# Optimization experiments

Measured on AMD Instinct MI355X. Metric: run time of the kernel, lower is better.

The kernel has to match this reference:

```python
import jax, jax.numpy as jnp
import numpy as np

B, S, D, H = 2, 2048, 1024, 16
HD = D // H  # head dim = 64


def setup_inputs() -> dict:
    key = jax.random.key(0)
    ks = jax.random.split(key, 11)
    s = 0.02
    return {
        "query": jax.random.normal(ks[0], (B, S, D), jnp.float32),
        "key": jax.random.normal(ks[1], (B, S, D), jnp.float32),
        "value": jax.random.normal(ks[2], (B, S, D), jnp.float32),
        "Wq": jax.random.normal(ks[3], (D, D), jnp.float32) * s,
        "bq": jnp.zeros((D,), jnp.float32),
        "Wk": jax.random.normal(ks[4], (D, D), jnp.float32) * s,
        "bk": jnp.zeros((D,), jnp.float32),
        "Wv": jax.random.normal(ks[5], (D, D), jnp.float32) * s,
        "bv": jnp.zeros((D,), jnp.float32),
        "Wo": jax.random.normal(ks[6], (D, D), jnp.float32) * s,
        "bo": jnp.zeros((D,), jnp.float32),
    }


def reference(query, key, value, Wq, bq, Wk, bk, Wv, bv, Wo, bo):
    # Linear projections (torch Linear: x @ W^T + b; here W stored as [in, out])
    q = query @ Wq + bq  # [B,S,D]
    k = key @ Wk + bk
    v = value @ Wv + bv
    # split heads -> [B,H,S,HD]
    q = q.reshape(B, S, H, HD).transpose(0, 2, 1, 3)
    k = k.reshape(B, S, H, HD).transpose(0, 2, 1, 3)
    v = v.reshape(B, S, H, HD).transpose(0, 2, 1, 3)
    scores = jnp.einsum("bhqd,bhkd->bhqk", q, k) / jnp.sqrt(jnp.float32(HD))
    probs = jax.nn.softmax(scores, axis=-1)
    # dropout is identity at inference
    ctx = jnp.einsum("bhqk,bhkd->bhqd", probs, v)
    ctx = ctx.transpose(0, 2, 1, 3).reshape(B, S, D)
    return ctx @ Wo + bo
```

## Files before the change

kernel.cpp:

```cpp
#include <hip/hip_runtime.h>
#include <hip/hip_bf16.h>

#define BB 2
#define SS 2048
#define DD 1024
#define HH 16
#define HD 64
#define MM (BB*SS)

typedef __attribute__((ext_vector_type(8))) short bf16x8;
typedef __attribute__((ext_vector_type(4))) float f32x4;

static __device__ inline unsigned short f2bf(float x) {
    unsigned int u = __float_as_uint(x);
    unsigned int r = (u + 0x7fffu + ((u >> 16) & 1u)) >> 16;
    return (unsigned short)r;
}

static __device__ inline unsigned pack2bf(float lo, float hi) {
    union { __hip_bfloat162 h; unsigned u; } c;
    c.h = __float22bfloat162_rn(make_float2(lo, hi));
    return c.u;
}

static __device__ inline f32x4 mfma16(bf16x8 a, bf16x8 b, f32x4 c) {
    return __builtin_amdgcn_mfma_f32_16x16x32_bf16(a, b, c, 0, 0, 0);
}

static __device__ inline float fast_exp2(float x) {
    return __builtin_amdgcn_exp2f(x);
}

typedef __attribute__((address_space(3))) unsigned int lds_u32;
typedef const __attribute__((address_space(1))) unsigned int glb_u32;
static __device__ inline void async_ld16(const void* g, void* l) {
    __builtin_amdgcn_global_load_lds((glb_u32*)g, (lds_u32*)l, 16, 0, 0);
}

struct PrepArgs {
    const float* csrc[3];
    unsigned short* cdst[3];
    const float* wsrc[4];
    unsigned short* wdst[4];
};
__global__ __launch_bounds__(256) void prep_inputs(PrepArgs args) {
    const int z = blockIdx.z;
    const int t = threadIdx.x;
    if (z < 3) {
        const float* in = args.csrc[z];
        unsigned short* out = args.cdst[z];
        int chunk = (blockIdx.y * 32 + blockIdx.x) * 4096;
#pragma unroll
        for (int r = 0; r < 4; r++) {
            int i = chunk + r * 1024 + t * 4;
            float4 v = *(const float4*)(in + i);
            uint2 o;
            o.x = pack2bf(v.x, v.y);
            o.y = pack2bf(v.z, v.w);
            *(uint2*)(out + i) = o;
        }
    } else {
        __shared__ float tile[32][33];
        const float* in = args.wsrc[z - 3];
        unsigned short* out = args.wdst[z - 3];
        int c0 = blockIdx.x * 32, r0 = blockIdx.y * 32;
        int x = t & 31, y0 = t >> 5;
        for (int yy = y0; yy < 32; yy += 8)
            tile[yy][x] = in[(size_t)(r0 + yy) * DD + c0 + x];
        __syncthreads();
        for (int yy = y0; yy < 32; yy += 8)
            out[(size_t)(c0 + yy) * DD + r0 + x] = f2bf(tile[x][yy]);
    }
}

struct QKVArgs {
    const unsigned short* A[3];
    const unsigned short* Bt[3];
    const float* bias[3];
    unsigned short* C[3];
};

#define QSCALE 0.1803368801111204f

#define NKT 16

__global__ __launch_bounds__(512, 2) void gemm_qkv(QKVArgs args) {
    __shared__ alignas(16) unsigned short AS[2][256 * 64];
    __shared__ alignas(16) unsigned short BS[2][256 * 64];
    const int z = blockIdx.z;
    const float scale = (z == 0) ? QSCALE : 1.0f;
    const unsigned short* __restrict__ A = args.A[z];
    const unsigned short* __restrict__ Bt = args.Bt[z];
    const float* __restrict__ bias = args.bias[z];
    unsigned short* __restrict__ C = args.C[z];
    const int K = DD, N = DD;
    const int t = threadIdx.x;
    const int lane = t & 63, wave = t >> 6;
    const int quad = lane >> 4, l15 = lane & 15;
    const int wm = wave & 1, wn = wave >> 1;
    const int m0 = blockIdx.y * 256, n0 = blockIdx.x * 256;

    const int srow = t >> 3;
    const int cslot = (t & 7) ^ (srow & 7);
    const unsigned short* gA = A + (size_t)(m0 + srow) * K + cslot * 8;
    const unsigned short* gB = Bt + (size_t)(n0 + srow) * K + cslot * 8;
    const int dstoff = srow * 64 + (t & 7) * 8;

    auto stageA = [&](int tl, int h) {
        unsigned short* d = &AS[tl & 1][h * 128 * 64 + dstoff];
        const unsigned short* s = gA + (size_t)(h * 128) * K + (size_t)tl * 64;
        async_ld16(s, d);
        async_ld16(s + (size_t)64 * K, d + 64 * 64);
    };
    auto stageB = [&](int tl, int h) {
        unsigned short* d = &BS[tl & 1][h * 128 * 64 + dstoff];
        const unsigned short* s = gB + (size_t)(h * 128) * K + (size_t)tl * 64;
        async_ld16(s, d);
        async_ld16(s + (size_t)64 * K, d + 64 * 64);
    };

    stageA(0, 0); stageA(0, 1); stageB(0, 0); stageB(0, 1);
    stageA(1, 0); stageA(1, 1);

    f32x4 acc[8][4];
#pragma unroll
    for (int i = 0; i < 8; i++)
#pragma unroll
        for (int j = 0; j < 4; j++) acc[i][j] = (f32x4){0.f, 0.f, 0.f, 0.f};

#pragma unroll 2
    for (int kt = 0; kt < NKT; ++kt) {
        if (kt < NKT - 1) asm volatile("s_waitcnt vmcnt(4)" ::: "memory");
        else              asm volatile("s_waitcnt vmcnt(0)" ::: "memory");
        __builtin_amdgcn_s_barrier();

        const unsigned short* Ab = AS[kt & 1];
        const unsigned short* Bb = BS[kt & 1];
        bf16x8 af[4][2], bf[4][2];

#pragma unroll
        for (int i = 0; i < 4; i++) {
            const int row = wm * 128 + i * 16 + l15;
#pragma unroll
            for (int kk = 0; kk < 2; kk++)
                af[i][kk] = *(const bf16x8*)&Ab[row * 64 + ((kk * 4 + quad) ^ (l15 & 7)) * 8];
        }
#pragma unroll
        for (int j = 0; j < 2; j++) {
            const int row = wn * 64 + j * 16 + l15;
#pragma unroll
            for (int kk = 0; kk < 2; kk++)
                bf[j][kk] = *(const bf16x8*)&Bb[row * 64 + ((kk * 4 + quad) ^ (l15 & 7)) * 8];
        }
        if (kt + 1 < NKT) stageB(kt + 1, 0);
        __builtin_amdgcn_s_barrier();
        __builtin_amdgcn_s_setprio(1);
#pragma unroll
        for (int i = 0; i < 4; i++)
#pragma unroll
            for (int j = 0; j < 2; j++) {
                acc[i][j] = mfma16(af[i][0], bf[j][0], acc[i][j]);
                acc[i][j] = mfma16(af[i][1], bf[j][1], acc[i][j]);
            }
        __builtin_amdgcn_s_setprio(0);
        __builtin_amdgcn_s_barrier();

#pragma unroll
        for (int j = 2; j < 4; j++) {
            const int row = wn * 64 + j * 16 + l15;
#pragma unroll
            for (int kk = 0; kk < 2; kk++)
                bf[j][kk] = *(const bf16x8*)&Bb[row * 64 + ((kk * 4 + quad) ^ (l15 & 7)) * 8];
        }
        if (kt + 1 < NKT) stageB(kt + 1, 1);
        __builtin_amdgcn_s_barrier();
        __builtin_amdgcn_s_setprio(1);
#pragma unroll
        for (int i = 0; i < 4; i++)
#pragma unroll
            for (int j = 2; j < 4; j++) {
                acc[i][j] = mfma16(af[i][0], bf[j][0], acc[i][j]);
                acc[i][j] = mfma16(af[i][1], bf[j][1], acc[i][j]);
            }
        __builtin_amdgcn_s_setprio(0);
        __builtin_amdgcn_s_barrier();

#pragma unroll
        for (int i = 0; i < 4; i++) {
            const int row = wm * 128 + 64 + i * 16 + l15;
#pragma unroll
            for (int kk = 0; kk < 2; kk++)
                af[i][kk] = *(const bf16x8*)&Ab[row * 64 + ((kk * 4 + quad) ^ (l15 & 7)) * 8];
        }
        __builtin_amdgcn_s_barrier();
        __builtin_amdgcn_s_setprio(1);
#pragma unroll
        for (int i = 0; i < 4; i++)
#pragma unroll
            for (int j = 0; j < 2; j++) {
                acc[4 + i][j] = mfma16(af[i][0], bf[j][0], acc[4 + i][j]);
                acc[4 + i][j] = mfma16(af[i][1], bf[j][1], acc[4 + i][j]);
            }
        __builtin_amdgcn_s_setprio(0);
        __builtin_amdgcn_s_barrier();

        if (kt + 2 < NKT) { stageA(kt + 2, 0); stageA(kt + 2, 1); }
        __builtin_amdgcn_s_barrier();
        __builtin_amdgcn_s_setprio(1);
#pragma unroll
        for (int i = 0; i < 4; i++)
#pragma unroll
            for (int j = 2; j < 4; j++) {
                acc[4 + i][j] = mfma16(af[i][0], bf[j][0], acc[4 + i][j]);
                acc[4 + i][j] = mfma16(af[i][1], bf[j][1], acc[4 + i][j]);
            }
        __builtin_amdgcn_s_setprio(0);
    }

    if (z == 2) {
#pragma unroll
        for (int j = 0; j < 4; j++) {
            int col = n0 + wn * 64 + j * 16 + l15;
            float bv = bias[col];
#pragma unroll
            for (int i = 0; i < 8; i++) {
                int rowb = m0 + wm * 128 + i * 16 + quad * 4;
                int b = rowb >> 11, s = rowb & (SS - 1);
                uint2 w;
                w.x = pack2bf(acc[i][j][0] + bv, acc[i][j][1] + bv);
                w.y = pack2bf(acc[i][j][2] + bv, acc[i][j][3] + bv);
                *(uint2*)(C + (size_t)b * DD * SS + (size_t)col * SS + s) = w;
            }
        }
    } else {
#pragma unroll
        for (int j = 0; j < 4; j++) {
            int col = n0 + wn * 64 + j * 16 + l15;
            float bv = bias[col];
#pragma unroll
            for (int i = 0; i < 8; i++) {
                int rowb = m0 + wm * 128 + i * 16 + quad * 4;
#pragma unroll
                for (int rr = 0; rr < 4; rr++) {
                    float v = (acc[i][j][rr] + bv) * scale;
                    C[(size_t)(rowb + rr) * N + col] = f2bf(v);
                }
            }
        }
    }
}

#define ONKT 16

__global__ __launch_bounds__(256, 2) void gemm_out(const unsigned short* __restrict__ A,
                                                   const unsigned short* __restrict__ Bt,
                                                   const float* __restrict__ bias,
                                                   float* __restrict__ C) {
    __shared__ alignas(16) unsigned short AS[2][128 * 64];
    __shared__ alignas(16) unsigned short BS[2][128 * 64];
    const int t = threadIdx.x;
    const int lane = t & 63, wave = t >> 6;
    const int quad = lane >> 4, l15 = lane & 15;
    const int wm = wave & 1, wn = wave >> 1;
    const int m0 = blockIdx.y * 128, n0 = blockIdx.x * 128;
    const int K = DD, N = DD;

    const int srow = t >> 3;
    const int cslot = (t & 7) ^ (srow & 7);
    const unsigned short* gA = A + (size_t)(m0 + srow) * K + cslot * 8;
    const unsigned short* gB = Bt + (size_t)(n0 + srow) * K + cslot * 8;
    const int dstoff = srow * 64 + (t & 7) * 8;

    auto stageA = [&](int tl) {
        unsigned short* d = &AS[tl & 1][dstoff];
        const unsigned short* s = gA + (size_t)tl * 64;
#pragma unroll
        for (int r = 0; r < 4; r++)
            async_ld16(s + (size_t)(r * 32) * K, d + r * 32 * 64);
    };
    auto stageB = [&](int tl) {
        unsigned short* d = &BS[tl & 1][dstoff];
        const unsigned short* s = gB + (size_t)tl * 64;
#pragma unroll
        for (int r = 0; r < 4; r++)
            async_ld16(s + (size_t)(r * 32) * K, d + r * 32 * 64);
    };

    stageA(0); stageB(0); stageA(1);

    f32x4 acc[4][4];
#pragma unroll
    for (int i = 0; i < 4; i++)
#pragma unroll
        for (int j = 0; j < 4; j++) acc[i][j] = (f32x4){0.f, 0.f, 0.f, 0.f};

#pragma unroll 2
    for (int kt = 0; kt < ONKT; ++kt) {
        if (kt < ONKT - 1) asm volatile("s_waitcnt vmcnt(4)" ::: "memory");
        else               asm volatile("s_waitcnt vmcnt(0)" ::: "memory");
        __builtin_amdgcn_s_barrier();

        const unsigned short* Ab = AS[kt & 1];
        const unsigned short* Bb = BS[kt & 1];
        bf16x8 af[4][2], bf[4][2];

#pragma unroll
        for (int i = 0; i < 4; i++) {
            const int row = wm * 64 + i * 16 + l15;
#pragma unroll
            for (int kk = 0; kk < 2; kk++)
                af[i][kk] = *(const bf16x8*)&Ab[row * 64 + ((kk * 4 + quad) ^ (l15 & 7)) * 8];
        }
#pragma unroll
        for (int j = 0; j < 2; j++) {
            const int row = wn * 64 + j * 16 + l15;
#pragma unroll
            for (int kk = 0; kk < 2; kk++)
                bf[j][kk] = *(const bf16x8*)&Bb[row * 64 + ((kk * 4 + quad) ^ (l15 & 7)) * 8];
        }
        if (kt + 1 < ONKT) stageB(kt + 1);
        __builtin_amdgcn_s_barrier();
        __builtin_amdgcn_s_setprio(1);
#pragma unroll
        for (int i = 0; i < 4; i++)
#pragma unroll
            for (int j = 0; j < 2; j++) {
                acc[i][j] = mfma16(af[i][0], bf[j][0], acc[i][j]);
                acc[i][j] = mfma16(af[i][1], bf[j][1], acc[i][j]);
            }
        __builtin_amdgcn_s_setprio(0);
        __builtin_amdgcn_s_barrier();

#pragma unroll
        for (int j = 2; j < 4; j++) {
            const int row = wn * 64 + j * 16 + l15;
#pragma unroll
            for (int kk = 0; kk < 2; kk++)
                bf[j][kk] = *(const bf16x8*)&Bb[row * 64 + ((kk * 4 + quad) ^ (l15 & 7)) * 8];
        }
        if (kt + 2 < ONKT) stageA(kt + 2);
        __builtin_amdgcn_s_barrier();
        __builtin_amdgcn_s_setprio(1);
#pragma unroll
        for (int i = 0; i < 4; i++)
#pragma unroll
            for (int j = 2; j < 4; j++) {
                acc[i][j] = mfma16(af[i][0], bf[j][0], acc[i][j]);
                acc[i][j] = mfma16(af[i][1], bf[j][1], acc[i][j]);
            }
        __builtin_amdgcn_s_setprio(0);
    }

#pragma unroll
    for (int j = 0; j < 4; j++) {
        int col = n0 + wn * 64 + j * 16 + l15;
        float bv = bias[col];
#pragma unroll
        for (int i = 0; i < 4; i++) {
            int rowb = m0 + wm * 64 + i * 16 + quad * 4;
#pragma unroll
            for (int rr = 0; rr < 4; rr++)
                C[(size_t)(rowb + rr) * N + col] = acc[i][j][rr] + bv;
        }
    }
}

#define TK 64
#define NTILE (SS / TK)
#define LDP 72

__global__ __launch_bounds__(256, 2) void flash_attn(const unsigned short* __restrict__ Q,
                                                     const unsigned short* __restrict__ Kg,
                                                     const unsigned short* __restrict__ Vt,
                                                     unsigned short* __restrict__ ctx) {
    __shared__ alignas(16) unsigned short Ks[2][TK * LDP];
    __shared__ alignas(16) unsigned short Vs[2][TK * LDP];
    const int t = threadIdx.x;
    const int lane = t & 63, wave = t >> 6;
    const int quad = lane >> 4, l15 = lane & 15;
    const int qg = blockIdx.x & 15;
    const int bh = blockIdx.x >> 4;
    const int h = bh & 15, b = bh >> 4;
    const int q0 = (qg * 4 + wave) * 32;

    const unsigned short* Qb = Q + (size_t)b * SS * DD + h * HD;
    const unsigned short* Kb = Kg + (size_t)b * SS * DD + h * HD;
    const unsigned short* Vb = Vt + ((size_t)b * DD + h * HD) * SS;

    const int r0 = t >> 3, cs = t & 7;
    const unsigned short* gK = Kb + (size_t)r0 * DD + cs * 8;
    const unsigned short* gV = Vb + (size_t)r0 * SS + cs * 8;
    const int ldsoff0 = r0 * LDP + cs * 8;
    const int ldsoff1 = (r0 + 32) * LDP + cs * 8;

    bf16x8 qa[2][2];
#pragma unroll
    for (int qt = 0; qt < 2; qt++) {
        qa[qt][0] = *(const bf16x8*)(Qb + (size_t)(q0 + qt * 16 + l15) * DD + quad * 8);
        qa[qt][1] = *(const bf16x8*)(Qb + (size_t)(q0 + qt * 16 + l15) * DD + 32 + quad * 8);
    }

    float lrow[2] = {0.f, 0.f};
    f32x4 o[2][4];
#pragma unroll
    for (int qt = 0; qt < 2; qt++)
#pragma unroll
        for (int j = 0; j < 4; j++) o[qt][j] = (f32x4){0.f, 0.f, 0.f, 0.f};

    {
        uint4 kr0 = *(const uint4*)(gK);
        uint4 kr1 = *(const uint4*)(gK + (size_t)32 * DD);
        uint4 vr0 = *(const uint4*)(gV);
        uint4 vr1 = *(const uint4*)(gV + (size_t)32 * SS);
        *(uint4*)&Ks[0][ldsoff0] = kr0;
        *(uint4*)&Ks[0][ldsoff1] = kr1;
        *(uint4*)&Vs[0][ldsoff0] = vr0;
        *(uint4*)&Vs[0][ldsoff1] = vr1;
    }
    __syncthreads();

    for (int tile = 0; tile < NTILE; ++tile) {
        const int buf = tile & 1;
        uint4 kr0, kr1, vr0, vr1;
        if (tile + 1 < NTILE) {
            const unsigned short* gKn = gK + (size_t)(tile + 1) * TK * DD;
            const unsigned short* gVn = gV + (tile + 1) * TK;
            kr0 = *(const uint4*)(gKn);
            kr1 = *(const uint4*)(gKn + (size_t)32 * DD);
            vr0 = *(const uint4*)(gVn);
            vr1 = *(const uint4*)(gVn + (size_t)32 * SS);
        }
        const unsigned short* Ksb = Ks[buf];
        const unsigned short* Vsb = Vs[buf];
#pragma unroll
        for (int half = 0; half < 2; half++) {
            const int kb0 = half * 32;
            bf16x8 k0 = *(const bf16x8*)&Ksb[(kb0 + l15) * LDP + quad * 8];
            bf16x8 k1 = *(const bf16x8*)&Ksb[(kb0 + l15) * LDP + 32 + quad * 8];
            bf16x8 k2 = *(const bf16x8*)&Ksb[(kb0 + 16 + l15) * LDP + quad * 8];
            bf16x8 k3 = *(const bf16x8*)&Ksb[(kb0 + 16 + l15) * LDP + 32 + quad * 8];
            union { ushort4 s[2]; bf16x8 v; } af[4];
#pragma unroll
            for (int j = 0; j < 4; j++) {
                af[j].s[0] = *(const ushort4*)&Vsb[(j * 16 + l15) * LDP + kb0 + quad * 4];
                af[j].s[1] = *(const ushort4*)&Vsb[(j * 16 + l15) * LDP + kb0 + 16 + quad * 4];
            }
#pragma unroll
            for (int qt = 0; qt < 2; qt++) {
                f32x4 sc0 = (f32x4){0.f, 0.f, 0.f, 0.f};
                f32x4 sc1 = (f32x4){0.f, 0.f, 0.f, 0.f};
                sc0 = mfma16(k0, qa[qt][0], sc0);
                sc0 = mfma16(k1, qa[qt][1], sc0);
                sc1 = mfma16(k2, qa[qt][0], sc1);
                sc1 = mfma16(k3, qa[qt][1], sc1);

                float p[8];
#pragma unroll
                for (int rr = 0; rr < 4; rr++) {
                    p[rr]     = fast_exp2(sc0[rr]);
                    p[rr + 4] = fast_exp2(sc1[rr]);
                }
                lrow[qt] += (p[0] + p[1]) + (p[2] + p[3]) + (p[4] + p[5]) + (p[6] + p[7]);

                union { unsigned u[4]; bf16x8 v; } pf;
                pf.u[0] = pack2bf(p[0], p[1]);
                pf.u[1] = pack2bf(p[2], p[3]);
                pf.u[2] = pack2bf(p[4], p[5]);
                pf.u[3] = pack2bf(p[6], p[7]);

#pragma unroll
                for (int j = 0; j < 4; j++)
                    o[qt][j] = mfma16(af[j].v, pf.v, o[qt][j]);
            }
        }
        if (tile + 1 < NTILE) {
            __syncthreads();
            *(uint4*)&Ks[buf ^ 1][ldsoff0] = kr0;
            *(uint4*)&Ks[buf ^ 1][ldsoff1] = kr1;
            *(uint4*)&Vs[buf ^ 1][ldsoff0] = vr0;
            *(uint4*)&Vs[buf ^ 1][ldsoff1] = vr1;
            __syncthreads();
        }
    }

#pragma unroll
    for (int qt = 0; qt < 2; qt++) {
        float l = lrow[qt];
        l += __shfl_xor(l, 16, 64);
        l += __shfl_xor(l, 32, 64);
        float linv = 1.0f / l;
        unsigned short* crow = ctx + ((size_t)b * SS + q0 + qt * 16 + l15) * DD + h * HD;
#pragma unroll
        for (int j = 0; j < 4; j++) {
            uint2 w;
            w.x = pack2bf(o[qt][j][0] * linv, o[qt][j][1] * linv);
            w.y = pack2bf(o[qt][j][2] * linv, o[qt][j][3] * linv);
            *(uint2*)(crow + j * 16 + quad * 4) = w;
        }
    }
}

extern "C" void kernel_launch(void* const* d_in, const int* in_sizes, int n_in,
                              void* d_out, int out_size, void* d_ws, size_t ws_size,
                              hipStream_t stream) {
    const float* query = (const float*)d_in[0];
    const float* key   = (const float*)d_in[1];
    const float* value = (const float*)d_in[2];
    const float* Wq = (const float*)d_in[3];
    const float* bq = (const float*)d_in[4];
    const float* Wk = (const float*)d_in[5];
    const float* bk = (const float*)d_in[6];
    const float* Wv = (const float*)d_in[7];
    const float* bv = (const float*)d_in[8];
    const float* Wo = (const float*)d_in[9];
    const float* bo = (const float*)d_in[10];
    float* out = (float*)d_out;

    char* ws = (char*)d_ws;
    const size_t WSZ = (size_t)DD * DD * 2;
    const size_t XSZ = (size_t)MM * DD * 2;
    unsigned short* Wqt = (unsigned short*)(ws + 0 * WSZ);
    unsigned short* Wkt = (unsigned short*)(ws + 1 * WSZ);
    unsigned short* Wvt = (unsigned short*)(ws + 2 * WSZ);
    unsigned short* Wot = (unsigned short*)(ws + 3 * WSZ);
    unsigned short* Xq  = (unsigned short*)(ws + 4 * WSZ);
    unsigned short* Xk  = (unsigned short*)(ws + 4 * WSZ + 1 * XSZ);
    unsigned short* Xv  = (unsigned short*)(ws + 4 * WSZ + 2 * XSZ);
    unsigned short* Qp  = (unsigned short*)(ws + 4 * WSZ + 3 * XSZ);
    unsigned short* Kp  = (unsigned short*)(ws + 4 * WSZ + 4 * XSZ);
    unsigned short* Vtp = (unsigned short*)(ws + 4 * WSZ + 5 * XSZ);
    unsigned short* ctx = Xk;

    PrepArgs pargs;
    pargs.csrc[0] = query; pargs.csrc[1] = key; pargs.csrc[2] = value;
    pargs.cdst[0] = Xq; pargs.cdst[1] = Xk; pargs.cdst[2] = Xv;
    pargs.wsrc[0] = Wq; pargs.wsrc[1] = Wk; pargs.wsrc[2] = Wv; pargs.wsrc[3] = Wo;
    pargs.wdst[0] = Wqt; pargs.wdst[1] = Wkt; pargs.wdst[2] = Wvt; pargs.wdst[3] = Wot;
    prep_inputs<<<dim3(32, 32, 7), 256, 0, stream>>>(pargs);

    QKVArgs args;
    args.A[0] = Xq; args.A[1] = Xk; args.A[2] = Xv;
    args.Bt[0] = Wqt; args.Bt[1] = Wkt; args.Bt[2] = Wvt;
    args.bias[0] = bq; args.bias[1] = bk; args.bias[2] = bv;
    args.C[0] = Qp; args.C[1] = Kp; args.C[2] = Vtp;
    gemm_qkv<<<dim3(DD / 256, MM / 256, 3), 512, 0, stream>>>(args);

    flash_attn<<<BB * HH * 16, 256, 0, stream>>>(Qp, Kp, Vtp, ctx);

    gemm_out<<<dim3(DD / 128, MM / 128), 256, 0, stream>>>(ctx, Wot, bo, out);
}
```

Baseline: 229.5 us.

## Fuse fp32-to-bf16 activation conversion into QKV GEMM and triple-buffer attention K/V

The QKV GEMM now reads fp32 activations directly through registers, converts them to bf16 and writes them to LDS, so the separate conversion pass and its bf16 intermediate buffers are gone. The weight prep kernel is simplified to use vectorized float4 loads and packed stores. Flash attention moves from two to three LDS buffers for K/V, which drops one of the two barriers per tile. This removes a full read/write round trip of the activations, at the cost of twice the global A bytes, a register-staged A load in the GEMM, and more LDS use in attention, which may lower occupancy.

```diff
diff --git a/kernel.cpp b/kernel.cpp
--- a/kernel.cpp
+++ b/kernel.cpp
@@ -38,43 +38,36 @@
 }
 
 struct PrepArgs {
-    const float* csrc[3];
-    unsigned short* cdst[3];
     const float* wsrc[4];
     unsigned short* wdst[4];
 };
 __global__ __launch_bounds__(256) void prep_inputs(PrepArgs args) {
+    __shared__ float tile[32][33];
     const int z = blockIdx.z;
     const int t = threadIdx.x;
-    if (z < 3) {
-        const float* in = args.csrc[z];
-        unsigned short* out = args.cdst[z];
-        int chunk = (blockIdx.y * 32 + blockIdx.x) * 4096;
-#pragma unroll
-        for (int r = 0; r < 4; r++) {
-            int i = chunk + r * 1024 + t * 4;
-            float4 v = *(const float4*)(in + i);
-            uint2 o;
-            o.x = pack2bf(v.x, v.y);
-            o.y = pack2bf(v.z, v.w);
-            *(uint2*)(out + i) = o;
-        }
-    } else {
-        __shared__ float tile[32][33];
-        const float* in = args.wsrc[z - 3];
-        unsigned short* out = args.wdst[z - 3];
-        int c0 = blockIdx.x * 32, r0 = blockIdx.y * 32;
-        int x = t & 31, y0 = t >> 5;
-        for (int yy = y0; yy < 32; yy += 8)
-            tile[yy][x] = in[(size_t)(r0 + yy) * DD + c0 + x];
-        __syncthreads();
-        for (int yy = y0; yy < 32; yy += 8)
-            out[(size_t)(c0 + yy) * DD + r0 + x] = f2bf(tile[x][yy]);
+    const float* in = args.wsrc[z];
+    unsigned short* out = args.wdst[z];
+    const int c0 = blockIdx.x * 32, r0 = blockIdx.y * 32;
+    {
+        const int xf = (t & 7) * 4, yf = t >> 3;
+        float4 v = *(const float4*)(in + (size_t)(r0 + yf) * DD + c0 + xf);
+        tile[yf][xf + 0] = v.x;
+        tile[yf][xf + 1] = v.y;
+        tile[yf][xf + 2] = v.z;
+        tile[yf][xf + 3] = v.w;
+    }
+    __syncthreads();
+    {
+        const int x8 = t & 7, y8 = t >> 3;
+        uint2 w;
+        w.x = pack2bf(tile[x8 * 4 + 0][y8], tile[x8 * 4 + 1][y8]);
+        w.y = pack2bf(tile[x8 * 4 + 2][y8], tile[x8 * 4 + 3][y8]);
+        *(uint2*)(out + (size_t)(c0 + y8) * DD + r0 + x8 * 4) = w;
     }
 }
 
 struct QKVArgs {
-    const unsigned short* A[3];
+    const float* Af[3];
     const unsigned short* Bt[3];
     const float* bias[3];
     unsigned short* C[3];
@@ -89,7 +82,7 @@
     __shared__ alignas(16) unsigned short BS[2][256 * 64];
     const int z = blockIdx.z;
     const float scale = (z == 0) ? QSCALE : 1.0f;
-    const unsigned short* __restrict__ A = args.A[z];
+    const float* __restrict__ Af = args.Af[z];
     const unsigned short* __restrict__ Bt = args.Bt[z];
     const float* __restrict__ bias = args.bias[z];
     unsigned short* __restrict__ C = args.C[z];
@@ -102,16 +95,9 @@
 
     const int srow = t >> 3;
     const int cslot = (t & 7) ^ (srow & 7);
-    const unsigned short* gA = A + (size_t)(m0 + srow) * K + cslot * 8;
     const unsigned short* gB = Bt + (size_t)(n0 + srow) * K + cslot * 8;
     const int dstoff = srow * 64 + (t & 7) * 8;
 
-    auto stageA = [&](int tl, int h) {
-        unsigned short* d = &AS[tl & 1][h * 128 * 64 + dstoff];
-        const unsigned short* s = gA + (size_t)(h * 128) * K + (size_t)tl * 64;
-        async_ld16(s, d);
-        async_ld16(s + (size_t)64 * K, d + 64 * 64);
-    };
     auto stageB = [&](int tl, int h) {
         unsigned short* d = &BS[tl & 1][h * 128 * 64 + dstoff];
         const unsigned short* s = gB + (size_t)(h * 128) * K + (size_t)tl * 64;
@@ -119,8 +105,46 @@
         async_ld16(s + (size_t)64 * K, d + 64 * 64);
     };
 
-    stageA(0, 0); stageA(0, 1); stageB(0, 0); stageB(0, 1);
-    stageA(1, 0); stageA(1, 1);
+    const int ar_ = t >> 3, as_ = t & 7;
+    const int sw = as_ ^ (ar_ & 7);
+    const float* gA0 = Af + (size_t)(m0 + 0 * 64 + ar_) * K + sw * 8;
+    const float* gA1 = Af + (size_t)(m0 + 1 * 64 + ar_) * K + sw * 8;
+    const float* gA2 = Af + (size_t)(m0 + 2 * 64 + ar_) * K + sw * 8;
+    const float* gA3 = Af + (size_t)(m0 + 3 * 64 + ar_) * K + sw * 8;
+
+    float4 fA0[8], fA1[8];
+#define ISSUE_A(buf_, tl_)                                                    \
+    {                                                                         \
+        const size_t ko_ = (size_t)(tl_) * 64;                                \
+        buf_[0] = *(const float4*)(gA0 + ko_);                                \
+        buf_[1] = *(const float4*)(gA0 + ko_ + 4);                            \
+        buf_[2] = *(const float4*)(gA1 + ko_);                                \
+        buf_[3] = *(const float4*)(gA1 + ko_ + 4);                            \
+        buf_[4] = *(const float4*)(gA2 + ko_);                                \
+        buf_[5] = *(const float4*)(gA2 + ko_ + 4);                            \
+        buf_[6] = *(const float4*)(gA3 + ko_);                                \
+        buf_[7] = *(const float4*)(gA3 + ko_ + 4);                            \
+    }
+#define CVT_WRITE_A(buf_, tl_)                                                \
+    {                                                                         \
+        _Pragma("unroll")                                                     \
+        for (int h = 0; h < 4; h++) {                                         \
+            uint4 w_;                                                         \
+            w_.x = pack2bf(buf_[h * 2].x, buf_[h * 2].y);                     \
+            w_.y = pack2bf(buf_[h * 2].z, buf_[h * 2].w);                     \
+            w_.z = pack2bf(buf_[h * 2 + 1].x, buf_[h * 2 + 1].y);             \
+            w_.w = pack2bf(buf_[h * 2 + 1].z, buf_[h * 2 + 1].w);             \
+            *(uint4*)&AS[(tl_) & 1][(h * 64 + ar_) * 64 + as_ * 8] = w_;      \
+        }                                                                     \
+    }
+
+    ISSUE_A(fA0, 0);
+    stageB(0, 0); stageB(0, 1);
+    ISSUE_A(fA1, 1);
+    asm volatile("s_waitcnt vmcnt(8)" ::: "memory");
+    CVT_WRITE_A(fA0, 0);
+    asm volatile("s_waitcnt lgkmcnt(0)" ::: "memory");
+    __builtin_amdgcn_s_barrier();
 
     f32x4 acc[8][4];
 #pragma unroll
@@ -130,9 +154,11 @@
 
 #pragma unroll 2
     for (int kt = 0; kt < NKT; ++kt) {
-        if (kt < NKT - 1) asm volatile("s_waitcnt vmcnt(4)" ::: "memory");
-        else              asm volatile("s_waitcnt vmcnt(0)" ::: "memory");
-        __builtin_amdgcn_s_barrier();
+        if (kt > 0) {
+            if (kt < NKT - 1) asm volatile("s_waitcnt vmcnt(8) lgkmcnt(0)" ::: "memory");
+            else              asm volatile("s_waitcnt vmcnt(0) lgkmcnt(0)" ::: "memory");
+            __builtin_amdgcn_s_barrier();
+        }
 
         const unsigned short* Ab = AS[kt & 1];
         const unsigned short* Bb = BS[kt & 1];
@@ -152,7 +178,7 @@
             for (int kk = 0; kk < 2; kk++)
                 bf[j][kk] = *(const bf16x8*)&Bb[row * 64 + ((kk * 4 + quad) ^ (l15 & 7)) * 8];
         }
-        if (kt + 1 < NKT) stageB(kt + 1, 0);
+        if (kt + 1 < NKT) { stageB(kt + 1, 0); stageB(kt + 1, 1); }
         __builtin_amdgcn_s_barrier();
         __builtin_amdgcn_s_setprio(1);
 #pragma unroll
@@ -172,7 +198,6 @@
             for (int kk = 0; kk < 2; kk++)
                 bf[j][kk] = *(const bf16x8*)&Bb[row * 64 + ((kk * 4 + quad) ^ (l15 & 7)) * 8];
         }
-        if (kt + 1 < NKT) stageB(kt + 1, 1);
         __builtin_amdgcn_s_barrier();
         __builtin_amdgcn_s_setprio(1);
 #pragma unroll
@@ -204,7 +229,10 @@
         __builtin_amdgcn_s_setprio(0);
         __builtin_amdgcn_s_barrier();
 
-        if (kt + 2 < NKT) { stageA(kt + 2, 0); stageA(kt + 2, 1); }
+        if (kt + 1 < NKT) {
+            CVT_WRITE_A(fA1, kt + 1);
+            if (kt + 2 < NKT) ISSUE_A(fA1, kt + 2);
+        }
         __builtin_amdgcn_s_barrier();
         __builtin_amdgcn_s_setprio(1);
 #pragma unroll
@@ -248,6 +276,8 @@
             }
         }
     }
+#undef ISSUE_A
+#undef CVT_WRITE_A
 }
 
 #define ONKT 16
@@ -373,8 +403,8 @@
                                                      const unsigned short* __restrict__ Kg,
                                                      const unsigned short* __restrict__ Vt,
                                                      unsigned short* __restrict__ ctx) {
-    __shared__ alignas(16) unsigned short Ks[2][TK * LDP];
-    __shared__ alignas(16) unsigned short Vs[2][TK * LDP];
+    __shared__ alignas(16) unsigned short Ks[3][TK * LDP];
+    __shared__ alignas(16) unsigned short Vs[3][TK * LDP];
     const int t = threadIdx.x;
     const int lane = t & 63, wave = t >> 6;
     const int quad = lane >> 4, l15 = lane & 15;
@@ -419,8 +449,8 @@
     }
     __syncthreads();
 
+    int rb = 0;
     for (int tile = 0; tile < NTILE; ++tile) {
-        const int buf = tile & 1;
         uint4 kr0, kr1, vr0, vr1;
         if (tile + 1 < NTILE) {
             const unsigned short* gKn = gK + (size_t)(tile + 1) * TK * DD;
@@ -430,8 +460,8 @@
             vr0 = *(const uint4*)(gVn);
             vr1 = *(const uint4*)(gVn + (size_t)32 * SS);
         }
-        const unsigned short* Ksb = Ks[buf];
-        const unsigned short* Vsb = Vs[buf];
+        const unsigned short* Ksb = Ks[rb];
+        const unsigned short* Vsb = Vs[rb];
 #pragma unroll
         for (int half = 0; half < 2; half++) {
             const int kb0 = half * 32;
@@ -474,12 +504,13 @@
             }
         }
         if (tile + 1 < NTILE) {
+            int wb = rb + 1; if (wb == 3) wb = 0;
+            *(uint4*)&Ks[wb][ldsoff0] = kr0;
+            *(uint4*)&Ks[wb][ldsoff1] = kr1;
+            *(uint4*)&Vs[wb][ldsoff0] = vr0;
+            *(uint4*)&Vs[wb][ldsoff1] = vr1;
             __syncthreads();
-            *(uint4*)&Ks[buf ^ 1][ldsoff0] = kr0;
-            *(uint4*)&Ks[buf ^ 1][ldsoff1] = kr1;
-            *(uint4*)&Vs[buf ^ 1][ldsoff0] = vr0;
-            *(uint4*)&Vs[buf ^ 1][ldsoff1] = vr1;
-            __syncthreads();
+            rb = wb;
         }
     }
 
@@ -523,23 +554,18 @@
     unsigned short* Wkt = (unsigned short*)(ws + 1 * WSZ);
     unsigned short* Wvt = (unsigned short*)(ws + 2 * WSZ);
     unsigned short* Wot = (unsigned short*)(ws + 3 * WSZ);
-    unsigned short* Xq  = (unsigned short*)(ws + 4 * WSZ);
-    unsigned short* Xk  = (unsigned short*)(ws + 4 * WSZ + 1 * XSZ);
-    unsigned short* Xv  = (unsigned short*)(ws + 4 * WSZ + 2 * XSZ);
-    unsigned short* Qp  = (unsigned short*)(ws + 4 * WSZ + 3 * XSZ);
-    unsigned short* Kp  = (unsigned short*)(ws + 4 * WSZ + 4 * XSZ);
-    unsigned short* Vtp = (unsigned short*)(ws + 4 * WSZ + 5 * XSZ);
-    unsigned short* ctx = Xk;
+    unsigned short* Qp  = (unsigned short*)(ws + 4 * WSZ + 0 * XSZ);
+    unsigned short* Kp  = (unsigned short*)(ws + 4 * WSZ + 1 * XSZ);
+    unsigned short* Vtp = (unsigned short*)(ws + 4 * WSZ + 2 * XSZ);
+    unsigned short* ctx = (unsigned short*)(ws + 4 * WSZ + 3 * XSZ);
 
     PrepArgs pargs;
-    pargs.csrc[0] = query; pargs.csrc[1] = key; pargs.csrc[2] = value;
-    pargs.cdst[0] = Xq; pargs.cdst[1] = Xk; pargs.cdst[2] = Xv;
     pargs.wsrc[0] = Wq; pargs.wsrc[1] = Wk; pargs.wsrc[2] = Wv; pargs.wsrc[3] = Wo;
     pargs.wdst[0] = Wqt; pargs.wdst[1] = Wkt; pargs.wdst[2] = Wvt; pargs.wdst[3] = Wot;
-    prep_inputs<<<dim3(32, 32, 7), 256, 0, stream>>>(pargs);
+    prep_inputs<<<dim3(32, 32, 4), 256, 0, stream>>>(pargs);
 
     QKVArgs args;
-    args.A[0] = Xq; args.A[1] = Xk; args.A[2] = Xv;
+    args.Af[0] = query; args.Af[1] = key; args.Af[2] = value;
     args.Bt[0] = Wqt; args.Bt[1] = Wkt; args.Bt[2] = Wvt;
     args.bias[0] = bq; args.bias[1] = bk; args.bias[2] = bv;
     args.C[0] = Qp; args.C[1] = Kp; args.C[2] = Vtp;
```

New measurement: 225.0 us. About the same (-2.0%).
